# Performance work log

Measured on AMD Instinct MI355X. Metric: run time of the kernel, lower is better.

Reference implementation:

```python
import jax, jax.numpy as jnp
import numpy as np

N = 50000   # nodes
E = 800000  # edges (avg degree 16)
D = 128     # in_features == out_features (residual)
NEG_SLOPE = 0.2
BN_EPS = 1e-5


def setup_inputs() -> dict:
    key = jax.random.key(0)
    ks = jax.random.split(key, 8)
    x = jax.random.normal(ks[0], (N, D), jnp.float32)
    edge_index = jax.random.randint(ks[1], (2, E), 0, N, dtype=jnp.int32)
    W = jax.random.normal(ks[2], (D, D), jnp.float32) * 0.05
    att_src = jax.random.normal(ks[3], (D,), jnp.float32) * 0.1
    att_dst = jax.random.normal(ks[4], (D,), jnp.float32) * 0.1
    bias = jax.random.normal(ks[5], (D,), jnp.float32) * 0.01
    gamma = jnp.ones((D,), jnp.float32) + jax.random.normal(ks[6], (D,), jnp.float32) * 0.05
    beta = jax.random.normal(ks[7], (D,), jnp.float32) * 0.05
    return {"x": x, "edge_index": edge_index, "W": W, "att_src": att_src,
            "att_dst": att_dst, "bias": bias, "gamma": gamma, "beta": beta}


def reference(x, edge_index, W, att_src, att_dst, bias, gamma, beta):
    src, dst = edge_index[0], edge_index[1]
    # Linear transform (GATConv lin)
    h = x @ W                                   # [N, D]
    # Per-node attention logit halves
    a_s = h @ att_src                           # [N]
    a_d = h @ att_dst                           # [N]
    # Per-edge logits + LeakyReLU
    e = jax.nn.leaky_relu(a_s[src] + a_d[dst], NEG_SLOPE)  # [E]
    # Segment softmax over destination neighborhoods
    m = jax.ops.segment_max(e, dst, num_segments=N)        # [N]
    m = jnp.where(jnp.isfinite(m), m, 0.0)
    p = jnp.exp(e - m[dst])                                 # [E]
    denom = jax.ops.segment_sum(p, dst, num_segments=N)    # [N]
    alpha = p / denom[dst]                                  # [E]
    # Scatter-aggregate weighted neighbor features
    y = jax.ops.segment_sum(alpha[:, None] * h[src], dst, num_segments=N)  # [N, D]
    y = y + bias
    # NormDropRes (eval mode): BN with running_mean=0, running_var=1; dropout off
    yn = gamma * (y / jnp.sqrt(1.0 + BN_EPS)) + beta
    yn = jax.nn.relu(yn)
    # residual: in==out so base = x
    return x + yn
```

## Files before the change

### kernel.cpp

```cpp
#include <hip/hip_runtime.h>
#include <math.h>

#define NN 50000
#define EE 800000
#define DD 128
#define NEG 0.2f
#define SLOT 48
#define NWIN 128
#define WIN 391
#define CAP 7168
#define QW 98

typedef short bf16x8 __attribute__((ext_vector_type(8)));
typedef float f32x4  __attribute__((ext_vector_type(4)));
typedef int   i32x4  __attribute__((ext_vector_type(4)));

__device__ __forceinline__ unsigned short f2bf(float f) {
    unsigned u = __float_as_uint(f);
    unsigned r = u + 0x7fffu + ((u >> 16) & 1u);
    return (unsigned short)(r >> 16);
}

__global__ __launch_bounds__(256) void k_pre(
        const float* __restrict__ W, unsigned short* __restrict__ wt,
        int* __restrict__ win_cnt)
{
    const int t = threadIdx.x;
    if (blockIdx.x == 64) {
        if (t < NWIN) win_cnt[t] = 0;
        return;
    }
    int idx = blockIdx.x * 256 + t;
    int k = idx >> 7, n = idx & 127;
    wt[n * DD + k] = f2bf(W[idx]);
}

#define XS_STRIDE 136
__global__ __launch_bounds__(256) void k_A(
        const float* __restrict__ x, const unsigned short* __restrict__ wtg,
        const float* __restrict__ att_src, const float* __restrict__ att_dst,
        unsigned short* __restrict__ hb, float* __restrict__ a_s, float* __restrict__ a_d,
        const int* __restrict__ ei, int* __restrict__ win_cnt, unsigned* __restrict__ pairs)
{
    __shared__ __align__(16) short smem[26112];
    const int t = threadIdx.x;

    if (blockIdx.x & 1) {
        int* lcnt  = (int*)smem;
        int* lbase = (int*)smem + NWIN;
        if (t < NWIN) lcnt[t] = 0;
        __syncthreads();

        int idx = (int)(blockIdx.x >> 1) * 256 + t;
        int b[4], lp[4];
        unsigned v[4];
        bool valid = idx < EE / 4;
        if (valid) {
            i32x4 s4 = __builtin_nontemporal_load(&((const i32x4*)ei)[idx]);
            i32x4 d4 = __builtin_nontemporal_load(&((const i32x4*)(ei + EE))[idx]);
            b[0] = d4.x / WIN; v[0] = ((unsigned)(d4.x - b[0] * WIN) << 16) | (unsigned)s4.x;
            b[1] = d4.y / WIN; v[1] = ((unsigned)(d4.y - b[1] * WIN) << 16) | (unsigned)s4.y;
            b[2] = d4.z / WIN; v[2] = ((unsigned)(d4.z - b[2] * WIN) << 16) | (unsigned)s4.z;
            b[3] = d4.w / WIN; v[3] = ((unsigned)(d4.w - b[3] * WIN) << 16) | (unsigned)s4.w;
            lp[0] = atomicAdd(&lcnt[b[0]], 1);
            lp[1] = atomicAdd(&lcnt[b[1]], 1);
            lp[2] = atomicAdd(&lcnt[b[2]], 1);
            lp[3] = atomicAdd(&lcnt[b[3]], 1);
        }
        __syncthreads();
        if (t < NWIN) lbase[t] = atomicAdd(&win_cnt[t], lcnt[t]);
        __syncthreads();
        if (valid) {
#pragma unroll
            for (int k = 0; k < 4; k++) {
                int pos = lbase[b[k]] + lp[k];
                if (pos < CAP) pairs[(size_t)b[k] * CAP + pos] = v[k];
            }
        }
        return;
    }

    short* xs = smem;
    short* ws = smem + 64 * XS_STRIDE;
    const int row0 = (int)(blockIdx.x >> 1) * 64;

#pragma unroll
    for (int i = 0; i < 4; i++) {
        int idx = t + i * 256;
        int m = idx >> 4, c = idx & 15;
        int row = row0 + m;
        float4 f0 = make_float4(0.f, 0.f, 0.f, 0.f), f1 = f0;
        if (row < NN) {
            const float* p = x + (size_t)row * DD + c * 8;
            f0 = *(const float4*)p;
            f1 = *(const float4*)(p + 4);
        }
        bf16x8 v;
        v[0] = (short)f2bf(f0.x); v[1] = (short)f2bf(f0.y);
        v[2] = (short)f2bf(f0.z); v[3] = (short)f2bf(f0.w);
        v[4] = (short)f2bf(f1.x); v[5] = (short)f2bf(f1.y);
        v[6] = (short)f2bf(f1.z); v[7] = (short)f2bf(f1.w);
        *(bf16x8*)&xs[m * XS_STRIDE + c * 8] = v;
    }
#pragma unroll
    for (int i = 0; i < 8; i++) {
        int idx = t + i * 256;
        int n = idx >> 4, c = idx & 15;
        uint4 v = ((const uint4*)wtg)[idx];
        *(uint4*)&ws[n * XS_STRIDE + c * 8] = v;
    }
    __syncthreads();

    const int wv = t >> 6;
    const int lane = t & 63;
    const int n0 = lane & 15;
    const int quad = lane >> 4;

    bf16x8 afr[4];
#pragma unroll
    for (int kc = 0; kc < 4; kc++)
        afr[kc] = *(const bf16x8*)&xs[(wv * 16 + n0) * XS_STRIDE + kc * 32 + quad * 8];

    f32x4 acc[8];
#pragma unroll
    for (int nt = 0; nt < 8; nt++) {
        f32x4 a = {0.f, 0.f, 0.f, 0.f};
#pragma unroll
        for (int kc = 0; kc < 4; kc++) {
            bf16x8 bfr = *(const bf16x8*)&ws[(nt * 16 + n0) * XS_STRIDE + kc * 32 + quad * 8];
            a = __builtin_amdgcn_mfma_f32_16x16x32_bf16(afr[kc], bfr, a, 0, 0, 0);
        }
        acc[nt] = a;
    }

    const int rbase = row0 + wv * 16 + quad * 4;
    float ss[4] = {0.f, 0.f, 0.f, 0.f};
    float sd[4] = {0.f, 0.f, 0.f, 0.f};
#pragma unroll
    for (int nt = 0; nt < 8; nt++) {
        int col = nt * 16 + n0;
        float asc = att_src[col], adc = att_dst[col];
#pragma unroll
        for (int r = 0; r < 4; r++) {
            float v = acc[nt][r];
            ss[r] = fmaf(v, asc, ss[r]);
            sd[r] = fmaf(v, adc, sd[r]);
            int row = rbase + r;
            if (row < NN) hb[(size_t)row * DD + col] = f2bf(v);
        }
    }
#pragma unroll
    for (int r = 0; r < 4; r++) {
#pragma unroll
        for (int off = 1; off < 16; off <<= 1) {
            ss[r] += __shfl_xor(ss[r], off);
            sd[r] += __shfl_xor(sd[r], off);
        }
    }
    if (n0 == 0) {
#pragma unroll
        for (int r = 0; r < 4; r++) {
            int row = rbase + r;
            if (row < NN) { a_s[row] = ss[r]; a_d[row] = sd[r]; }
        }
    }
}

__global__ __launch_bounds__(512) void k_BN(
        const int* __restrict__ win_cnt, const unsigned* __restrict__ pairs,
        const float* __restrict__ a_s, const float* __restrict__ a_d,
        const unsigned short* __restrict__ hb, const float* __restrict__ x,
        const float* __restrict__ bias, const float* __restrict__ gamma,
        const float* __restrict__ beta, float* __restrict__ out)
{
    __shared__ int lcur[QW];
    __shared__ __align__(16) unsigned short lslots[QW * SLOT];
    const int t = threadIdx.x;
    const int w = (int)(blockIdx.x >> 2);
    const int q = (int)(blockIdx.x & 3);
    const int lo = q * QW;
    int hi = lo + QW; if (hi > WIN) hi = WIN;
    const int nloc = hi - lo;

    for (int i = t; i < QW; i += 512) lcur[i] = 0;
    __syncthreads();

    int n = win_cnt[w]; if (n > CAP) n = CAP;
    const unsigned* pw = pairs + (size_t)w * CAP;
    for (int g = t; g < n; g += 512) {
        unsigned v = pw[g];
        int ld = (int)(v >> 16);
        if (ld >= lo && ld < hi) {
            int pos = atomicAdd(&lcur[ld - lo], 1);
            if (pos < SLOT) lslots[(ld - lo) * SLOT + pos] = (unsigned short)(v & 0xffffu);
        }
    }
    __syncthreads();

    const int wv = t >> 6;
    const int lane = t & 63;
    const int eq = lane >> 4;
    const int fl = lane & 15;
    const float invbn = 0.9999950000374997f;

    for (int nl = wv; nl < nloc; nl += 8) {
        int node = w * WIN + lo + nl;
        if (node >= NN) break;

        int deg = lcur[nl];
        deg = deg > SLOT ? SLOT : deg;
        float ad = a_d[node];

        int s = 0;
        float p = 0.f;
        if (lane < deg) {
            s = (int)lslots[nl * SLOT + lane];
            float e = a_s[s] + ad;
            e = e > 0.f ? e : NEG * e;
            p = __expf(e);
        }
        float l = p;
#pragma unroll
        for (int off = 32; off > 0; off >>= 1)
            l += __shfl_xor(l, off);

        float acc[8];
#pragma unroll
        for (int k = 0; k < 8; k++) acc[k] = 0.f;

        for (int tt = 0; tt < deg; tt += 8) {
            int i0 = tt + eq, i1 = tt + 4 + eq;
            int   st0 = __shfl(s, i0);
            int   st1 = __shfl(s, i1);
            float pt0 = __shfl(p, i0);
            float pt1 = __shfl(p, i1);
            uint4 hv0 = *(const uint4*)(hb + ((size_t)st0 << 7) + fl * 8);
            uint4 hv1 = *(const uint4*)(hb + ((size_t)st1 << 7) + fl * 8);
            acc[0] = fmaf(pt0, __uint_as_float(hv0.x << 16),          acc[0]);
            acc[1] = fmaf(pt0, __uint_as_float(hv0.x & 0xffff0000u),  acc[1]);
            acc[2] = fmaf(pt0, __uint_as_float(hv0.y << 16),          acc[2]);
            acc[3] = fmaf(pt0, __uint_as_float(hv0.y & 0xffff0000u),  acc[3]);
            acc[4] = fmaf(pt0, __uint_as_float(hv0.z << 16),          acc[4]);
            acc[5] = fmaf(pt0, __uint_as_float(hv0.z & 0xffff0000u),  acc[5]);
            acc[6] = fmaf(pt0, __uint_as_float(hv0.w << 16),          acc[6]);
            acc[7] = fmaf(pt0, __uint_as_float(hv0.w & 0xffff0000u),  acc[7]);
            acc[0] = fmaf(pt1, __uint_as_float(hv1.x << 16),          acc[0]);
            acc[1] = fmaf(pt1, __uint_as_float(hv1.x & 0xffff0000u),  acc[1]);
            acc[2] = fmaf(pt1, __uint_as_float(hv1.y << 16),          acc[2]);
            acc[3] = fmaf(pt1, __uint_as_float(hv1.y & 0xffff0000u),  acc[3]);
            acc[4] = fmaf(pt1, __uint_as_float(hv1.z << 16),          acc[4]);
            acc[5] = fmaf(pt1, __uint_as_float(hv1.z & 0xffff0000u),  acc[5]);
            acc[6] = fmaf(pt1, __uint_as_float(hv1.w << 16),          acc[6]);
            acc[7] = fmaf(pt1, __uint_as_float(hv1.w & 0xffff0000u),  acc[7]);
        }

#pragma unroll
        for (int off = 16; off < 64; off <<= 1) {
#pragma unroll
            for (int k = 0; k < 8; k++)
                acc[k] += __shfl_xor(acc[k], off);
        }

        if (eq == 0) {
            float invl = (deg > 0) ? 1.f / l : 0.f;
            int c0 = fl * 8;
            const float* bp = bias  + c0;
            const float* gp = gamma + c0;
            const float* ep = beta  + c0;
            const float* xp = x + ((size_t)node << 7) + c0;
            float* op = out + ((size_t)node << 7) + c0;
            float4 o0, o1;
            float* oo[2] = {(float*)&o0, (float*)&o1};
#pragma unroll
            for (int k = 0; k < 8; k++) {
                float y  = acc[k] * invl + bp[k];
                float yn = gp[k] * (y * invbn) + ep[k];
                yn = yn > 0.f ? yn : 0.f;
                oo[k >> 2][k & 3] = xp[k] + yn;
            }
            *(float4*)op       = o0;
            *(float4*)(op + 4) = o1;
        }
    }
}

extern "C" void kernel_launch(void* const* d_in, const int* in_sizes, int n_in,
                              void* d_out, int out_size, void* d_ws, size_t ws_size,
                              hipStream_t stream)
{
    const float* x     = (const float*)d_in[0];
    const int*   ei    = (const int*)  d_in[1];
    const float* W     = (const float*)d_in[2];
    const float* att_s = (const float*)d_in[3];
    const float* att_d = (const float*)d_in[4];
    const float* bias  = (const float*)d_in[5];
    const float* gamma = (const float*)d_in[6];
    const float* beta  = (const float*)d_in[7];
    float* out = (float*)d_out;

    int*            win_cnt = (int*)d_ws;
    unsigned*       pairs   = (unsigned*)(win_cnt + NWIN);
    float*          a_sv    = (float*)(pairs + (size_t)NWIN * CAP);
    float*          a_dv    = a_sv + NN;
    unsigned short* wtg     = (unsigned short*)(a_dv + NN);
    unsigned short* hb      = wtg + DD * DD;

    k_pre <<<65, 256, 0, stream>>>(W, wtg, win_cnt);
    k_A   <<<2 * ((NN + 63) / 64), 256, 0, stream>>>(x, wtg, att_s, att_d, hb,
                                                     a_sv, a_dv, ei, win_cnt, pairs);
    k_BN  <<<4 * NWIN, 512, 0, stream>>>(win_cnt, pairs, a_sv, a_dv,
                                         hb, x, bias, gamma, beta, out);
}
```

Baseline: 153.3 us.

## Bucket edges into 512 finer windows so each aggregation block reads only its own window

Edges are now bucketed into 512 destination windows of 98 nodes instead of 128 windows of 391 nodes that four blocks each rescanned and filtered. Each aggregation block, now 1024 threads, reads only its own window's pairs, which removes the fourfold redundant read of the pair buffer. The binning pass now keeps 512 local counters and skips global atomics for empty bins. The trade-off is more global atomic targets and a per-window capacity of 2048 that could overflow on skewed degree distributions.

```diff
diff --git a/kernel.cpp b/kernel.cpp
--- a/kernel.cpp
+++ b/kernel.cpp
@@ -6,10 +6,9 @@
 #define DD 128
 #define NEG 0.2f
 #define SLOT 48
-#define NWIN 128
-#define WIN 391
-#define CAP 7168
-#define QW 98
+#define NWIN 512
+#define WIN 98
+#define CAP 2048
 
 typedef short bf16x8 __attribute__((ext_vector_type(8)));
 typedef float f32x4  __attribute__((ext_vector_type(4)));
@@ -27,7 +26,7 @@
 {
     const int t = threadIdx.x;
     if (blockIdx.x == 64) {
-        if (t < NWIN) win_cnt[t] = 0;
+        for (int i = t; i < NWIN; i += 256) win_cnt[i] = 0;
         return;
     }
     int idx = blockIdx.x * 256 + t;
@@ -48,7 +47,7 @@
     if (blockIdx.x & 1) {
         int* lcnt  = (int*)smem;
         int* lbase = (int*)smem + NWIN;
-        if (t < NWIN) lcnt[t] = 0;
+        for (int i = t; i < NWIN; i += 256) lcnt[i] = 0;
         __syncthreads();
 
         int idx = (int)(blockIdx.x >> 1) * 256 + t;
@@ -68,7 +67,10 @@
             lp[3] = atomicAdd(&lcnt[b[3]], 1);
         }
         __syncthreads();
-        if (t < NWIN) lbase[t] = atomicAdd(&win_cnt[t], lcnt[t]);
+        for (int i = t; i < NWIN; i += 256) {
+            int c = lcnt[i];
+            lbase[i] = c ? atomicAdd(&win_cnt[i], c) : 0;
+        }
         __syncthreads();
         if (valid) {
 #pragma unroll
@@ -166,34 +168,31 @@
     }
 }
 
-__global__ __launch_bounds__(512) void k_BN(
+__global__ __launch_bounds__(1024) void k_BN(
         const int* __restrict__ win_cnt, const unsigned* __restrict__ pairs,
         const float* __restrict__ a_s, const float* __restrict__ a_d,
         const unsigned short* __restrict__ hb, const float* __restrict__ x,
         const float* __restrict__ bias, const float* __restrict__ gamma,
         const float* __restrict__ beta, float* __restrict__ out)
 {
-    __shared__ int lcur[QW];
-    __shared__ __align__(16) unsigned short lslots[QW * SLOT];
+    __shared__ int lcur[WIN];
+    __shared__ __align__(16) unsigned short lslots[WIN * SLOT];
     const int t = threadIdx.x;
-    const int w = (int)(blockIdx.x >> 2);
-    const int q = (int)(blockIdx.x & 3);
-    const int lo = q * QW;
-    int hi = lo + QW; if (hi > WIN) hi = WIN;
-    const int nloc = hi - lo;
-
-    for (int i = t; i < QW; i += 512) lcur[i] = 0;
+    const int w = (int)blockIdx.x;
+    int nloc = NN - w * WIN;
+    if (nloc <= 0) return;
+    if (nloc > WIN) nloc = WIN;
+
+    for (int i = t; i < WIN; i += 1024) lcur[i] = 0;
     __syncthreads();
 
     int n = win_cnt[w]; if (n > CAP) n = CAP;
     const unsigned* pw = pairs + (size_t)w * CAP;
-    for (int g = t; g < n; g += 512) {
+    for (int g = t; g < n; g += 1024) {
         unsigned v = pw[g];
         int ld = (int)(v >> 16);
-        if (ld >= lo && ld < hi) {
-            int pos = atomicAdd(&lcur[ld - lo], 1);
-            if (pos < SLOT) lslots[(ld - lo) * SLOT + pos] = (unsigned short)(v & 0xffffu);
-        }
+        int pos = atomicAdd(&lcur[ld], 1);
+        if (pos < SLOT) lslots[ld * SLOT + pos] = (unsigned short)(v & 0xffffu);
     }
     __syncthreads();
 
@@ -203,9 +202,8 @@
     const int fl = lane & 15;
     const float invbn = 0.9999950000374997f;
 
-    for (int nl = wv; nl < nloc; nl += 8) {
-        int node = w * WIN + lo + nl;
-        if (node >= NN) break;
+    for (int nl = wv; nl < nloc; nl += 16) {
+        int node = w * WIN + nl;
 
         int deg = lcur[nl];
         deg = deg > SLOT ? SLOT : deg;
@@ -308,6 +306,6 @@
     k_pre <<<65, 256, 0, stream>>>(W, wtg, win_cnt);
     k_A   <<<2 * ((NN + 63) / 64), 256, 0, stream>>>(x, wtg, att_s, att_d, hb,
                                                      a_sv, a_dv, ei, win_cnt, pairs);
-    k_BN  <<<4 * NWIN, 512, 0, stream>>>(win_cnt, pairs, a_sv, a_dv,
-                                         hb, x, bias, gamma, beta, out);
-}
+    k_BN  <<<NWIN, 1024, 0, stream>>>(win_cnt, pairs, a_sv, a_dv,
+                                      hb, x, bias, gamma, beta, out);
+}
```

Result: no change. 155.2 us (+1.3%).
